# Performance work log

Measured on AMD Instinct MI355X. Metric: run time of the kernel, lower is better.

## Reference

```python
import jax, jax.numpy as jnp
import numpy as np

N_NODES = 10000
N_EDGES = 640000
D_FEAT = 128


def setup_inputs() -> dict:
    key = jax.random.key(0)
    k1, k2, k3, k4 = jax.random.split(key, 4)
    edge_feat = jax.random.normal(k1, (N_EDGES, D_FEAT), dtype=jnp.float32)
    node_feat = jax.random.normal(k2, (N_NODES, D_FEAT), dtype=jnp.float32)
    recv_idx = jax.random.randint(k3, (N_EDGES,), 0, N_NODES, dtype=jnp.int64 if jax.config.jax_enable_x64 else jnp.int32)
    W = jax.random.normal(k4, (2 * D_FEAT, D_FEAT), dtype=jnp.float32) * (1.0 / np.sqrt(2 * D_FEAT))
    b = jnp.zeros((D_FEAT,), dtype=jnp.float32)
    return {"edge_feat": edge_feat, "node_feat": node_feat, "recv_idx": recv_idx, "W": W, "b": b}


def reference(edge_feat, node_feat, recv_idx, W, b):
    # Unsorted segment sum: scatter-add edge features into receiver nodes. [E,d] -> [N,d]
    n_nodes = node_feat.shape[0]
    agg = jax.ops.segment_sum(edge_feat, recv_idx, num_segments=n_nodes)
    # Concat node features with aggregated received-edge features. [N, 2d]
    collected = jnp.concatenate([node_feat, agg], axis=-1)
    # node_model: Linear(2d -> d)
    return collected @ W + b
```

## Files before the change

kernel.cpp:

```cpp
#include <hip/hip_runtime.h>

#define N_NODES 10000
#define N_EDGES 640000
#define D_FEAT 128

#define WS_COUNTS 0
#define WS_START  16384
#define WS_CURSOR 32768
#define WS_SORTED 49152
#define WS_INTS_NEEDED (WS_SORTED + N_EDGES)

__global__ void zero_counts_kernel(int* __restrict__ counts) {
    int i = blockIdx.x * blockDim.x + threadIdx.x;
    if (i < N_NODES) counts[i] = 0;
}

__global__ void hist_kernel(const int* __restrict__ recv, int* __restrict__ counts) {
    int e = blockIdx.x * blockDim.x + threadIdx.x;
    if (e < N_EDGES) atomicAdd(&counts[recv[e]], 1);
}

__global__ __launch_bounds__(1024) void prefix_kernel(const int* __restrict__ counts,
                                                      int* __restrict__ start,
                                                      int* __restrict__ cursor) {
    __shared__ int buf[1024];
    __shared__ int carry;
    const int tid = threadIdx.x;
    if (tid == 0) carry = 0;
    __syncthreads();
    for (int base = 0; base < N_NODES; base += 1024) {
        const int c = carry;
        const int idx = base + tid;
        const int v = (idx < N_NODES) ? counts[idx] : 0;
        buf[tid] = v;
        __syncthreads();
        for (int off = 1; off < 1024; off <<= 1) {
            int t = (tid >= off) ? buf[tid - off] : 0;
            __syncthreads();
            buf[tid] += t;
            __syncthreads();
        }
        const int excl = buf[tid] - v + c;
        if (idx < N_NODES) { start[idx] = excl; cursor[idx] = excl; }
        __syncthreads();
        if (tid == 0) carry = c + buf[1023];
        __syncthreads();
    }
    if (tid == 0) start[N_NODES] = N_EDGES;
}

__global__ void reorder_kernel(const int* __restrict__ recv,
                               int* __restrict__ cursor,
                               int* __restrict__ sorted_eid) {
    int e = blockIdx.x * blockDim.x + threadIdx.x;
    if (e < N_EDGES) {
        int pos = atomicAdd(&cursor[recv[e]], 1);
        sorted_eid[pos] = e;
    }
}

__global__ __launch_bounds__(128) void gather_kernel(
        const float* __restrict__ edge_feat,
        const int* __restrict__ sorted_eid,
        const int* __restrict__ start,
        float* __restrict__ agg) {
    const int n = blockIdx.x;
    const int j = threadIdx.x;
    const int s = start[n];
    const int e_end = start[n + 1];
    float acc = 0.f;
    int i = s;
    for (; i + 4 <= e_end; i += 4) {
        const int e0 = sorted_eid[i + 0];
        const int e1 = sorted_eid[i + 1];
        const int e2 = sorted_eid[i + 2];
        const int e3 = sorted_eid[i + 3];
        const float v0 = edge_feat[(long)e0 * D_FEAT + j];
        const float v1 = edge_feat[(long)e1 * D_FEAT + j];
        const float v2 = edge_feat[(long)e2 * D_FEAT + j];
        const float v3 = edge_feat[(long)e3 * D_FEAT + j];
        acc += (v0 + v1) + (v2 + v3);
    }
    for (; i < e_end; ++i)
        acc += edge_feat[(long)sorted_eid[i] * D_FEAT + j];
    agg[(long)n * D_FEAT + j] = acc;
}

__global__ void zero_agg_kernel(float4* __restrict__ agg4, int n4) {
    int i = blockIdx.x * blockDim.x + threadIdx.x;
    if (i < n4) agg4[i] = float4{0.f, 0.f, 0.f, 0.f};
}

__global__ __launch_bounds__(256) void scatter_kernel(
        const float4* __restrict__ edge_feat4,
        const int* __restrict__ recv,
        float* __restrict__ agg) {
    long gid = (long)blockIdx.x * blockDim.x + threadIdx.x;
    int e  = (int)(gid >> 5);
    int c4 = (int)(gid & 31);
    if (e >= N_EDGES) return;
    int r = recv[e];
    float4 v = edge_feat4[(long)e * 32 + c4];
    float* dst = agg + (long)r * D_FEAT + c4 * 4;
    unsafeAtomicAdd(dst + 0, v.x);
    unsafeAtomicAdd(dst + 1, v.y);
    unsafeAtomicAdd(dst + 2, v.z);
    unsafeAtomicAdd(dst + 3, v.w);
}

#define NT 16
__global__ __launch_bounds__(128) void gemm_kernel(
        const float* __restrict__ node_feat,
        const float* __restrict__ agg,
        const float* __restrict__ W,
        const float* __restrict__ b,
        float* __restrict__ out) {
    __shared__ float coll[NT][2 * D_FEAT];
    const int n0 = blockIdx.x * NT;
    const int j  = threadIdx.x;

    #pragma unroll
    for (int i = 0; i < NT; ++i) {
        coll[i][j]          = node_feat[(long)(n0 + i) * D_FEAT + j];
        coll[i][D_FEAT + j] = agg[(long)(n0 + i) * D_FEAT + j];
    }
    __syncthreads();

    float acc[NT];
    const float bias = b[j];
    #pragma unroll
    for (int i = 0; i < NT; ++i) acc[i] = bias;

    for (int k = 0; k < 2 * D_FEAT; k += 4) {
        const float w0 = W[(long)(k + 0) * D_FEAT + j];
        const float w1 = W[(long)(k + 1) * D_FEAT + j];
        const float w2 = W[(long)(k + 2) * D_FEAT + j];
        const float w3 = W[(long)(k + 3) * D_FEAT + j];
        #pragma unroll
        for (int i = 0; i < NT; ++i) {
            float4 c = *(const float4*)&coll[i][k];
            acc[i] += c.x * w0 + c.y * w1 + c.z * w2 + c.w * w3;
        }
    }

    #pragma unroll
    for (int i = 0; i < NT; ++i)
        out[(long)(n0 + i) * D_FEAT + j] = acc[i];
}

extern "C" void kernel_launch(void* const* d_in, const int* in_sizes, int n_in,
                              void* d_out, int out_size, void* d_ws, size_t ws_size,
                              hipStream_t stream) {
    const float* edge_feat = (const float*)d_in[0];
    const float* node_feat = (const float*)d_in[1];
    const int*   recv      = (const int*)d_in[2];
    const float* W         = (const float*)d_in[3];
    const float* b         = (const float*)d_in[4];
    float* out = (float*)d_out;
    float* agg = out;

    if (ws_size >= (size_t)WS_INTS_NEEDED * sizeof(int)) {
        int* wsi    = (int*)d_ws;
        int* counts = wsi + WS_COUNTS;
        int* startp = wsi + WS_START;
        int* cursor = wsi + WS_CURSOR;
        int* sorted = wsi + WS_SORTED;

        zero_counts_kernel<<<(N_NODES + 255) / 256, 256, 0, stream>>>(counts);
        hist_kernel<<<(N_EDGES + 255) / 256, 256, 0, stream>>>(recv, counts);
        prefix_kernel<<<1, 1024, 0, stream>>>(counts, startp, cursor);
        reorder_kernel<<<(N_EDGES + 255) / 256, 256, 0, stream>>>(recv, cursor, sorted);
        gather_kernel<<<N_NODES, 128, 0, stream>>>(edge_feat, sorted, startp, agg);
    } else {
        const int n4 = N_NODES * D_FEAT / 4;
        zero_agg_kernel<<<(n4 + 255) / 256, 256, 0, stream>>>((float4*)agg, n4);
        const long scatter_threads = (long)N_EDGES * 32;
        scatter_kernel<<<(int)(scatter_threads / 256), 256, 0, stream>>>(
            (const float4*)edge_feat, recv, agg);
    }

    gemm_kernel<<<N_NODES / NT, 128, 0, stream>>>(node_feat, agg, W, b, out);
}
```

Baseline: 587.8 us.

## Vectorize gather with multi-wave edge split and use shuffle-based prefix scan

The gather kernel now assigns 8 groups of 32 lanes per node, each lane loading float4 chunks of edge rows. Partial sums are reduced in shared memory, which raises memory-level parallelism over the old one-float-per-thread serial loop. The prefix scan uses wave shuffles and a two-level reduction instead of a shared-memory Hillis-Steele scan with many barriers. The atomic scatter fallback is removed, so the code now assumes the workspace is always large enough.

Result: no change. 577.9 us (-1.7%).

```diff
diff --git a/kernel.cpp b/kernel.cpp
--- a/kernel.cpp
+++ b/kernel.cpp
@@ -23,28 +23,40 @@
 __global__ __launch_bounds__(1024) void prefix_kernel(const int* __restrict__ counts,
                                                       int* __restrict__ start,
                                                       int* __restrict__ cursor) {
-    __shared__ int buf[1024];
-    __shared__ int carry;
-    const int tid = threadIdx.x;
-    if (tid == 0) carry = 0;
+    __shared__ int wsum[16];
+    __shared__ int carry_s;
+    const int tid  = threadIdx.x;
+    const int lane = tid & 63;
+    const int wave = tid >> 6;
+    if (tid == 0) carry_s = 0;
     __syncthreads();
     for (int base = 0; base < N_NODES; base += 1024) {
-        const int c = carry;
         const int idx = base + tid;
         const int v = (idx < N_NODES) ? counts[idx] : 0;
-        buf[tid] = v;
+        int x = v;
+        #pragma unroll
+        for (int off = 1; off < 64; off <<= 1) {
+            int t = __shfl_up(x, off, 64);
+            if (lane >= off) x += t;
+        }
+        if (lane == 63) wsum[wave] = x;
         __syncthreads();
-        for (int off = 1; off < 1024; off <<= 1) {
-            int t = (tid >= off) ? buf[tid - off] : 0;
-            __syncthreads();
-            buf[tid] += t;
-            __syncthreads();
+        if (wave == 0) {
+            int ws = (lane < 16) ? wsum[lane] : 0;
+            #pragma unroll
+            for (int off = 1; off < 16; off <<= 1) {
+                int t = __shfl_up(ws, off, 64);
+                if (lane >= off) ws += t;
+            }
+            if (lane < 16) wsum[lane] = ws;
         }
-        const int excl = buf[tid] - v + c;
+        __syncthreads();
+        const int carry   = carry_s;
+        const int waveoff = (wave == 0) ? 0 : wsum[wave - 1];
+        const int excl    = carry + waveoff + x - v;
         if (idx < N_NODES) { start[idx] = excl; cursor[idx] = excl; }
         __syncthreads();
-        if (tid == 0) carry = c + buf[1023];
-        __syncthreads();
+        if (tid == 1023) carry_s = carry + wsum[15];
     }
     if (tid == 0) start[N_NODES] = N_EDGES;
 }
@@ -59,53 +71,36 @@
     }
 }
 
-__global__ __launch_bounds__(128) void gather_kernel(
-        const float* __restrict__ edge_feat,
+#define GW 8
+__global__ __launch_bounds__(256) void gather_kernel(
+        const float4* __restrict__ edge_feat4,
         const int* __restrict__ sorted_eid,
         const int* __restrict__ start,
-        float* __restrict__ agg) {
-    const int n = blockIdx.x;
-    const int j = threadIdx.x;
+        float4* __restrict__ agg4) {
+    __shared__ float4 red[GW][32];
+    const int n   = blockIdx.x;
+    const int tid = threadIdx.x;
+    const int l   = tid & 31;
+    const int w   = tid >> 5;
     const int s = start[n];
-    const int e_end = start[n + 1];
-    float acc = 0.f;
-    int i = s;
-    for (; i + 4 <= e_end; i += 4) {
-        const int e0 = sorted_eid[i + 0];
-        const int e1 = sorted_eid[i + 1];
-        const int e2 = sorted_eid[i + 2];
-        const int e3 = sorted_eid[i + 3];
-        const float v0 = edge_feat[(long)e0 * D_FEAT + j];
-        const float v1 = edge_feat[(long)e1 * D_FEAT + j];
-        const float v2 = edge_feat[(long)e2 * D_FEAT + j];
-        const float v3 = edge_feat[(long)e3 * D_FEAT + j];
-        acc += (v0 + v1) + (v2 + v3);
+    const int e = start[n + 1];
+    float4 acc = {0.f, 0.f, 0.f, 0.f};
+    for (int i = s + w; i < e; i += GW) {
+        const long eid = sorted_eid[i];
+        const float4 v = edge_feat4[eid * 32 + l];
+        acc.x += v.x; acc.y += v.y; acc.z += v.z; acc.w += v.w;
     }
-    for (; i < e_end; ++i)
-        acc += edge_feat[(long)sorted_eid[i] * D_FEAT + j];
-    agg[(long)n * D_FEAT + j] = acc;
-}
-
-__global__ void zero_agg_kernel(float4* __restrict__ agg4, int n4) {
-    int i = blockIdx.x * blockDim.x + threadIdx.x;
-    if (i < n4) agg4[i] = float4{0.f, 0.f, 0.f, 0.f};
-}
-
-__global__ __launch_bounds__(256) void scatter_kernel(
-        const float4* __restrict__ edge_feat4,
-        const int* __restrict__ recv,
-        float* __restrict__ agg) {
-    long gid = (long)blockIdx.x * blockDim.x + threadIdx.x;
-    int e  = (int)(gid >> 5);
-    int c4 = (int)(gid & 31);
-    if (e >= N_EDGES) return;
-    int r = recv[e];
-    float4 v = edge_feat4[(long)e * 32 + c4];
-    float* dst = agg + (long)r * D_FEAT + c4 * 4;
-    unsafeAtomicAdd(dst + 0, v.x);
-    unsafeAtomicAdd(dst + 1, v.y);
-    unsafeAtomicAdd(dst + 2, v.z);
-    unsafeAtomicAdd(dst + 3, v.w);
+    red[w][l] = acc;
+    __syncthreads();
+    if (w == 0) {
+        float4 r = red[0][l];
+        #pragma unroll
+        for (int k = 1; k < GW; ++k) {
+            const float4 t = red[k][l];
+            r.x += t.x; r.y += t.y; r.z += t.z; r.w += t.w;
+        }
+        agg4[(long)n * 32 + l] = r;
+    }
 }
 
 #define NT 16
@@ -138,7 +133,7 @@
         const float w3 = W[(long)(k + 3) * D_FEAT + j];
         #pragma unroll
         for (int i = 0; i < NT; ++i) {
-            float4 c = *(const float4*)&coll[i][k];
+            const float4 c = *(const float4*)&coll[i][k];
             acc[i] += c.x * w0 + c.y * w1 + c.z * w2 + c.w * w3;
         }
     }
@@ -159,25 +154,17 @@
     float* out = (float*)d_out;
     float* agg = out;
 
-    if (ws_size >= (size_t)WS_INTS_NEEDED * sizeof(int)) {
-        int* wsi    = (int*)d_ws;
-        int* counts = wsi + WS_COUNTS;
-        int* startp = wsi + WS_START;
-        int* cursor = wsi + WS_CURSOR;
-        int* sorted = wsi + WS_SORTED;
+    int* wsi    = (int*)d_ws;
+    int* counts = wsi + WS_COUNTS;
+    int* startp = wsi + WS_START;
+    int* cursor = wsi + WS_CURSOR;
+    int* sorted = wsi + WS_SORTED;
 
-        zero_counts_kernel<<<(N_NODES + 255) / 256, 256, 0, stream>>>(counts);
-        hist_kernel<<<(N_EDGES + 255) / 256, 256, 0, stream>>>(recv, counts);
-        prefix_kernel<<<1, 1024, 0, stream>>>(counts, startp, cursor);
-        reorder_kernel<<<(N_EDGES + 255) / 256, 256, 0, stream>>>(recv, cursor, sorted);
-        gather_kernel<<<N_NODES, 128, 0, stream>>>(edge_feat, sorted, startp, agg);
-    } else {
-        const int n4 = N_NODES * D_FEAT / 4;
-        zero_agg_kernel<<<(n4 + 255) / 256, 256, 0, stream>>>((float4*)agg, n4);
-        const long scatter_threads = (long)N_EDGES * 32;
-        scatter_kernel<<<(int)(scatter_threads / 256), 256, 0, stream>>>(
-            (const float4*)edge_feat, recv, agg);
-    }
-
+    zero_counts_kernel<<<(N_NODES + 255) / 256, 256, 0, stream>>>(counts);
+    hist_kernel<<<(N_EDGES + 255) / 256, 256, 0, stream>>>(recv, counts);
+    prefix_kernel<<<1, 1024, 0, stream>>>(counts, startp, cursor);
+    reorder_kernel<<<(N_EDGES + 255) / 256, 256, 0, stream>>>(recv, cursor, sorted);
+    gather_kernel<<<N_NODES, 256, 0, stream>>>(
+        (const float4*)edge_feat, sorted, startp, (float4*)agg);
     gemm_kernel<<<N_NODES / NT, 128, 0, stream>>>(node_feat, agg, W, b, out);
 }
```
